# Kernel tuning notes

Measured on AMD Instinct MI355X. Metric: run time of the kernel, lower is better.

The kernel has to match this reference:

```python
import jax, jax.numpy as jnp
import numpy as np

NC = 16       # class_nums
C = 128       # in_channel == EMBEND_DIM
NS = 8192     # support points
NQ = 30000    # query points
EPS = 1e-8


def setup_inputs() -> dict:
    key = jax.random.key(0)
    ks = jax.random.split(key, 7)
    support_features = jax.random.normal(ks[0], (NS, C), dtype=jnp.float32)
    support_labels = jax.random.randint(ks[1], (NS,), 0, NC)
    query_features = jax.random.normal(ks[2], (NQ, C), dtype=jnp.float32)
    # proj = Linear(2C+1 -> C) + ReLU + Linear(C -> 128)
    s1 = 1.0 / np.sqrt(2 * C + 1)
    W1 = jax.random.uniform(ks[3], (2 * C + 1, C), minval=-s1, maxval=s1, dtype=jnp.float32)
    b1 = jax.random.uniform(ks[4], (C,), minval=-s1, maxval=s1, dtype=jnp.float32)
    s2 = 1.0 / np.sqrt(C)
    W2 = jax.random.uniform(ks[5], (C, C), minval=-s2, maxval=s2, dtype=jnp.float32)
    b2 = jax.random.uniform(ks[6], (C,), minval=-s2, maxval=s2, dtype=jnp.float32)
    return {"support_features": support_features, "support_labels": support_labels,
            "query_features": query_features, "W1": W1, "b1": b1, "W2": W2, "b2": b2}


def _prototypes(support_features, support_labels):
    # fused scatter-mean replacing the per-class Python loop
    sums = jax.ops.segment_sum(support_features, support_labels, num_segments=NC)  # [Nc, C]
    counts = jax.ops.segment_sum(jnp.ones((support_features.shape[0],), support_features.dtype),
                                 support_labels, num_segments=NC)                   # [Nc]
    return jnp.where(counts[:, None] > 0, sums / jnp.maximum(counts, 1.0)[:, None], 0.0)


def reference(support_features, support_labels, query_features, W1, b1, W2, b2):
    protos = _prototypes(support_features, support_labels)                # [Nc, C]
    # MD_distance: cosine similarity between each query and each class prototype
    qn = query_features / jnp.maximum(jnp.linalg.norm(query_features, axis=-1, keepdims=True), EPS)
    pn = protos / jnp.maximum(jnp.linalg.norm(protos, axis=-1, keepdims=True), EPS)
    cos = jnp.einsum('qc,nc->qn', qn, pn)                                 # [Nq, Nc]
    # proj(cat([query, proto, cos], -1)) without materializing the [Nq,Nc,2C+1] concat:
    # split W1 rows into query part, proto part, and cos part.
    Wq, Wp, Wc = W1[:C], W1[C:2 * C], W1[2 * C]                           # [C,C],[C,C],[C]
    h = jax.nn.relu(jnp.einsum('qc,ch->qh', query_features, Wq)[:, None, :]
                    + jnp.einsum('nc,ch->nh', protos, Wp)[None, :, :]
                    + cos[:, :, None] * Wc[None, None, :]
                    + b1)                                                 # [Nq, Nc, C]
    similarity = jnp.einsum('qnh,ho->qno', h, W2) + b2                    # [Nq, Nc, 128]
    return similarity, cos[:, :, None]
```

## Files before the change

kernel.cpp:

```cpp
#include <hip/hip_runtime.h>

#define NQ_ 30000
#define NC_ 16
#define C_  128
#define NS_ 8192
#define QB  16
#define NBLK (NQ_/QB)

typedef __attribute__((ext_vector_type(4))) float  f32x4;
typedef __attribute__((ext_vector_type(8))) short  s16x8;

#define WS_PART  0
#define WS_PCNT  32768
#define WS_T     33024
#define WS_PACK  35072

__device__ inline short f2bf(float x){
  unsigned u = __float_as_uint(x);
  u += 0x7fffu + ((u >> 16) & 1u);
  return (short)(u >> 16);
}

__global__ __launch_bounds__(128) void protoA(const float* __restrict__ sf,
                                              const int* __restrict__ lbl,
                                              const float* __restrict__ W1,
                                              const float* __restrict__ W2,
                                              float* __restrict__ ws){
  const int b = blockIdx.x;
  const int t = threadIdx.x;
  if (b < 256){
    const int cls = b >> 4;
    const int ch  = b & 15;
    const int r0  = ch * (NS_/16);
    float s = 0.f; int cnt = 0;
    #pragma unroll 4
    for (int r = r0; r < r0 + NS_/16; ++r){
      if (lbl[r] == cls){ s += sf[(size_t)r*C_ + t]; ++cnt; }
    }
    ws[WS_PART + (cls*16 + ch)*C_ + t] = s;
    if (t == 0) ws[WS_PCNT + cls*16 + ch] = (float)cnt;
  } else {
    short* packo = (short*)(ws + WS_PACK);
    const int g0 = (b - 256)*1024 + t*8;
    const int gg = g0 & 16383;
    const int ln = (gg >> 3) & 63, ks = (gg >> 9) & 3, wvv = gg >> 11;
    const int kb = ks*32 + ((ln >> 4) & 3)*8;
    const int col = wvv*16 + (ln & 15);
    const float* src = (g0 < 16384) ? W2 : W1;
    s16x8 v;
    #pragma unroll
    for (int i = 0; i < 8; ++i) v[i] = f2bf(src[(size_t)(kb + i)*C_ + col]);
    *(s16x8*)&packo[g0] = v;
  }
}

__global__ __launch_bounds__(128) void protoB(const float* __restrict__ W1,
                                              const float* __restrict__ b1,
                                              float* __restrict__ ws){
  __shared__ float pr[C_];
  __shared__ float rns;
  const int n = blockIdx.x;
  const int h = threadIdx.x;
  float s = 0.f;
  #pragma unroll
  for (int ch = 0; ch < 16; ++ch) s += ws[WS_PART + (n*16 + ch)*C_ + h];
  float cnt = 0.f;
  #pragma unroll
  for (int ch = 0; ch < 16; ++ch) cnt += ws[WS_PCNT + n*16 + ch];
  const float pv = (cnt > 0.f) ? s / fmaxf(cnt, 1.f) : 0.f;
  pr[h] = pv;
  __syncthreads();
  if (h < 64){
    float q = pr[h]*pr[h] + pr[h+64]*pr[h+64];
    q += __shfl_xor(q, 1);  q += __shfl_xor(q, 2);  q += __shfl_xor(q, 4);
    q += __shfl_xor(q, 8);  q += __shfl_xor(q, 16); q += __shfl_xor(q, 32);
    if (h == 0) rns = 1.f / fmaxf(sqrtf(q), 1e-8f);
  }
  __syncthreads();
  {
    short* packo = (short*)(ws + WS_PACK);
    const int k = h;
    const int gg = ((k >> 5)*64 + ((k >> 3) & 3)*16 + n)*8 + (k & 7);
    packo[32768 + gg] = f2bf(pv * rns);
  }
  float acc = b1[h];
  #pragma unroll 8
  for (int c = 0; c < C_; ++c) acc = fmaf(pr[c], W1[(size_t)(C_ + c)*C_ + h], acc);
  ws[WS_T + n*C_ + h] = acc;
}

__global__ __launch_bounds__(256, 4) void fused_main(const float* __restrict__ qfeat,
                                                     const float* __restrict__ W1,
                                                     const float* __restrict__ b2,
                                                     const float* __restrict__ ws,
                                                     float* __restrict__ out){
  __shared__ __align__(16) char un[16384];
  __shared__ float qw[QB][132];
  __shared__ float tl16[NC_][132];
  __shared__ float cosl[QB][NC_];
  __shared__ float rqn[QB];
  __shared__ float wcl[C_];

  float (*qfs)[132] = (float(*)[132])un;
  short* hfrag = (short*)un;

  const int t    = threadIdx.x;
  const int lane = t & 63;
  const int wv   = t >> 6;
  const int fr   = lane & 15;
  const int fg   = lane >> 4;
  const int qbase = blockIdx.x * QB;
  float* out_cos = out + (size_t)NQ_ * NC_ * C_;
  const short* pack = (const short*)(ws + WS_PACK);

  {
    const int idx = t * 8, q = idx >> 7, c = idx & 127;
    *(f32x4*)&qfs[q][c]      = *(const f32x4*)(qfeat + (size_t)qbase*C_ + idx);
    *(f32x4*)&qfs[q][c+4]    = *(const f32x4*)(qfeat + (size_t)qbase*C_ + idx + 4);
    *(f32x4*)&tl16[q][c]     = *(const f32x4*)(ws + WS_T + idx);
    *(f32x4*)&tl16[q][c+4]   = *(const f32x4*)(ws + WS_T + idx + 4);
    if (t < 32) *(f32x4*)&wcl[t*4] = *(const f32x4*)(W1 + 2*C_*C_ + t*4);
  }
  __syncthreads();

  if (t < 128){
    int q = t >> 3; int c0 = (t & 7) * 16;
    float s = 0.f;
    #pragma unroll
    for (int m = 0; m < 16; ++m){ float v = qfs[q][c0+m]; s = fmaf(v, v, s); }
    s += __shfl_xor(s, 1); s += __shfl_xor(s, 2); s += __shfl_xor(s, 4);
    if ((t & 7) == 0) rqn[q] = 1.f / fmaxf(sqrtf(s), 1e-8f);
  }

  s16x8 qfr[4];
  #pragma unroll
  for (int ks = 0; ks < 4; ++ks){
    const int c0 = ks*32 + fg*8;
    f32x4 a = *(const f32x4*)&qfs[fr][c0];
    f32x4 b = *(const f32x4*)&qfs[fr][c0+4];
    s16x8 v;
    v[0]=f2bf(a[0]); v[1]=f2bf(a[1]); v[2]=f2bf(a[2]); v[3]=f2bf(a[3]);
    v[4]=f2bf(b[0]); v[5]=f2bf(b[1]); v[6]=f2bf(b[2]); v[7]=f2bf(b[3]);
    qfr[ks] = v;
  }
  s16x8 w2f[2][4];
  float b2v[2];
  #pragma unroll
  for (int j = 0; j < 2; ++j){
    const int tt = wv*2 + j;
    #pragma unroll
    for (int ks = 0; ks < 4; ++ks)
      w2f[j][ks] = *(const s16x8*)&pack[((tt*4 + ks)*64 + lane)*8];
    b2v[j] = b2[tt*16 + fr];
  }
  __syncthreads();

  #pragma unroll
  for (int j = 0; j < 2; ++j){
    const int tt = wv*2 + j;
    f32x4 dq = {0.f,0.f,0.f,0.f};
    #pragma unroll
    for (int ks = 0; ks < 4; ++ks)
      dq = __builtin_amdgcn_mfma_f32_16x16x32_bf16(qfr[ks],
             *(const s16x8*)&pack[16384 + ((tt*4 + ks)*64 + lane)*8], dq, 0,0,0);
    #pragma unroll
    for (int r = 0; r < 4; ++r) qw[fg*4 + r][tt*16 + fr] = dq[r];
  }
  if (wv == 0){
    f32x4 dc = {0.f,0.f,0.f,0.f};
    #pragma unroll
    for (int ks = 0; ks < 4; ++ks)
      dc = __builtin_amdgcn_mfma_f32_16x16x32_bf16(qfr[ks],
             *(const s16x8*)&pack[32768 + (ks*64 + lane)*8], dc, 0,0,0);
    #pragma unroll
    for (int r = 0; r < 4; ++r){
      const int q = fg*4 + r;
      const float cv = dc[r] * rqn[q];
      cosl[q][fr] = cv;
      out_cos[(size_t)(qbase + q)*NC_ + fr] = cv;
    }
  }
  __syncthreads();

  const int k0 = wv*32 + fg*8;
  const f32x4 t8a = *(const f32x4*)&tl16[fr][k0];
  const f32x4 t8b = *(const f32x4*)&tl16[fr][k0+4];
  const f32x4 w8a = *(const f32x4*)&wcl[k0];
  const f32x4 w8b = *(const f32x4*)&wcl[k0+4];

  #pragma unroll
  for (int chunk = 0; chunk < 4; ++chunk){
    const int q0 = chunk * 4;
    #pragma unroll
    for (int qq = 0; qq < 4; ++qq){
      const int q = q0 + qq;
      f32x4 qa = *(const f32x4*)&qw[q][k0];
      f32x4 qb = *(const f32x4*)&qw[q][k0+4];
      const float cv = cosl[q][fr];
      s16x8 hv;
      #pragma unroll
      for (int jj = 0; jj < 4; ++jj)
        hv[jj] = f2bf(fmaxf(fmaf(cv, w8a[jj], qa[jj] + t8a[jj]), 0.f));
      #pragma unroll
      for (int jj = 0; jj < 4; ++jj)
        hv[4+jj] = f2bf(fmaxf(fmaf(cv, w8b[jj], qb[jj] + t8b[jj]), 0.f));
      *(s16x8*)&hfrag[qq*2048 + wv*512 + lane*8] = hv;
    }
    __syncthreads();
    #pragma unroll
    for (int qq = 0; qq < 4; ++qq){
      const short* hb = &hfrag[qq*2048 + lane*8];
      s16x8 a0 = *(const s16x8*)&hb[0];
      s16x8 a1 = *(const s16x8*)&hb[512];
      s16x8 a2 = *(const s16x8*)&hb[1024];
      s16x8 a3 = *(const s16x8*)&hb[1536];
      const size_t qout = (size_t)(qbase + q0 + qq) * (NC_*C_);
      #pragma unroll
      for (int j = 0; j < 2; ++j){
        f32x4 acc = {b2v[j], b2v[j], b2v[j], b2v[j]};
        acc = __builtin_amdgcn_mfma_f32_16x16x32_bf16(a0, w2f[j][0], acc, 0,0,0);
        acc = __builtin_amdgcn_mfma_f32_16x16x32_bf16(a1, w2f[j][1], acc, 0,0,0);
        acc = __builtin_amdgcn_mfma_f32_16x16x32_bf16(a2, w2f[j][2], acc, 0,0,0);
        acc = __builtin_amdgcn_mfma_f32_16x16x32_bf16(a3, w2f[j][3], acc, 0,0,0);
        const int ocol = (wv*2 + j)*16 + fr;
        #pragma unroll
        for (int r = 0; r < 4; ++r)
          out[qout + (fg*4 + r)*C_ + ocol] = acc[r];
      }
    }
    __syncthreads();
  }
}

extern "C" void kernel_launch(void* const* d_in, const int* in_sizes, int n_in,
                              void* d_out, int out_size, void* d_ws, size_t ws_size,
                              hipStream_t stream){
  const float* sf  = (const float*)d_in[0];
  const int*   lbl = (const int*)  d_in[1];
  const float* qf  = (const float*)d_in[2];
  const float* W1  = (const float*)d_in[3];
  const float* b1  = (const float*)d_in[4];
  const float* W2  = (const float*)d_in[5];
  const float* b2  = (const float*)d_in[6];
  float* ws  = (float*)d_ws;
  float* out = (float*)d_out;

  protoA<<<288, 128, 0, stream>>>(sf, lbl, W1, W2, ws);
  protoB<<<NC_, 128, 0, stream>>>(W1, b1, ws);
  fused_main<<<NBLK, 256, 0, stream>>>(qf, W1, b2, ws, out);
}
```

Measured before the change: 88.39 us.

## Stage MFMA outputs in double-buffered LDS for coalesced vector stores

Each wave now builds its full-K A fragments for the second matmul directly in registers instead of exchanging h through shared memory. The accumulator tiles are written to a double-buffered LDS staging area, then written to global memory as contiguous 32-byte vector stores per thread, overlapping with compute of the next query pair. This targets the scattered scalar output stores that dominate this output-write-bound kernel. The larger shared footprint lowers the occupancy hint from 4 to 3 blocks per CU, and the h values are recomputed redundantly across waves.

```diff
diff --git a/kernel.cpp b/kernel.cpp
--- a/kernel.cpp
+++ b/kernel.cpp
@@ -89,20 +89,19 @@
   ws[WS_T + n*C_ + h] = acc;
 }
 
-__global__ __launch_bounds__(256, 4) void fused_main(const float* __restrict__ qfeat,
+__global__ __launch_bounds__(256, 3) void fused_main(const float* __restrict__ qfeat,
                                                      const float* __restrict__ W1,
                                                      const float* __restrict__ b2,
                                                      const float* __restrict__ ws,
                                                      float* __restrict__ out){
-  __shared__ __align__(16) char un[16384];
+  __shared__ __align__(16) float simb[2*2*16*132];
   __shared__ float qw[QB][132];
   __shared__ float tl16[NC_][132];
   __shared__ float cosl[QB][NC_];
   __shared__ float rqn[QB];
   __shared__ float wcl[C_];
 
-  float (*qfs)[132] = (float(*)[132])un;
-  short* hfrag = (short*)un;
+  float (*qfs)[132] = (float(*)[132])simb;
 
   const int t    = threadIdx.x;
   const int lane = t & 63;
@@ -182,54 +181,69 @@
   }
   __syncthreads();
 
-  const int k0 = wv*32 + fg*8;
-  const f32x4 t8a = *(const f32x4*)&tl16[fr][k0];
-  const f32x4 t8b = *(const f32x4*)&tl16[fr][k0+4];
-  const f32x4 w8a = *(const f32x4*)&wcl[k0];
-  const f32x4 w8b = *(const f32x4*)&wcl[k0+4];
-
-  #pragma unroll
-  for (int chunk = 0; chunk < 4; ++chunk){
-    const int q0 = chunk * 4;
-    #pragma unroll
-    for (int qq = 0; qq < 4; ++qq){
-      const int q = q0 + qq;
-      f32x4 qa = *(const f32x4*)&qw[q][k0];
-      f32x4 qb = *(const f32x4*)&qw[q][k0+4];
+  auto do_C = [&](int p){
+    float* sb = simb + (p & 1) * (2*16*132);
+    #pragma unroll
+    for (int qq = 0; qq < 2; ++qq){
+      const int q = p*2 + qq;
       const float cv = cosl[q][fr];
-      s16x8 hv;
+      s16x8 af[4];
       #pragma unroll
-      for (int jj = 0; jj < 4; ++jj)
-        hv[jj] = f2bf(fmaxf(fmaf(cv, w8a[jj], qa[jj] + t8a[jj]), 0.f));
-      #pragma unroll
-      for (int jj = 0; jj < 4; ++jj)
-        hv[4+jj] = f2bf(fmaxf(fmaf(cv, w8b[jj], qb[jj] + t8b[jj]), 0.f));
-      *(s16x8*)&hfrag[qq*2048 + wv*512 + lane*8] = hv;
-    }
-    __syncthreads();
-    #pragma unroll
-    for (int qq = 0; qq < 4; ++qq){
-      const short* hb = &hfrag[qq*2048 + lane*8];
-      s16x8 a0 = *(const s16x8*)&hb[0];
-      s16x8 a1 = *(const s16x8*)&hb[512];
-      s16x8 a2 = *(const s16x8*)&hb[1024];
-      s16x8 a3 = *(const s16x8*)&hb[1536];
-      const size_t qout = (size_t)(qbase + q0 + qq) * (NC_*C_);
+      for (int ks = 0; ks < 4; ++ks){
+        const int k0 = ks*32 + fg*8;
+        const f32x4 qa = *(const f32x4*)&qw[q][k0];
+        const f32x4 qb = *(const f32x4*)&qw[q][k0+4];
+        const f32x4 ta = *(const f32x4*)&tl16[fr][k0];
+        const f32x4 tb = *(const f32x4*)&tl16[fr][k0+4];
+        const f32x4 wa = *(const f32x4*)&wcl[k0];
+        const f32x4 wb = *(const f32x4*)&wcl[k0+4];
+        s16x8 v;
+        #pragma unroll
+        for (int jj = 0; jj < 4; ++jj)
+          v[jj]   = f2bf(fmaxf(fmaf(cv, wa[jj], qa[jj] + ta[jj]), 0.f));
+        #pragma unroll
+        for (int jj = 0; jj < 4; ++jj)
+          v[4+jj] = f2bf(fmaxf(fmaf(cv, wb[jj], qb[jj] + tb[jj]), 0.f));
+        af[ks] = v;
+      }
       #pragma unroll
       for (int j = 0; j < 2; ++j){
         f32x4 acc = {b2v[j], b2v[j], b2v[j], b2v[j]};
-        acc = __builtin_amdgcn_mfma_f32_16x16x32_bf16(a0, w2f[j][0], acc, 0,0,0);
-        acc = __builtin_amdgcn_mfma_f32_16x16x32_bf16(a1, w2f[j][1], acc, 0,0,0);
-        acc = __builtin_amdgcn_mfma_f32_16x16x32_bf16(a2, w2f[j][2], acc, 0,0,0);
-        acc = __builtin_amdgcn_mfma_f32_16x16x32_bf16(a3, w2f[j][3], acc, 0,0,0);
+        acc = __builtin_amdgcn_mfma_f32_16x16x32_bf16(af[0], w2f[j][0], acc, 0,0,0);
+        acc = __builtin_amdgcn_mfma_f32_16x16x32_bf16(af[1], w2f[j][1], acc, 0,0,0);
+        acc = __builtin_amdgcn_mfma_f32_16x16x32_bf16(af[2], w2f[j][2], acc, 0,0,0);
+        acc = __builtin_amdgcn_mfma_f32_16x16x32_bf16(af[3], w2f[j][3], acc, 0,0,0);
         const int ocol = (wv*2 + j)*16 + fr;
         #pragma unroll
         for (int r = 0; r < 4; ++r)
-          out[qout + (fg*4 + r)*C_ + ocol] = acc[r];
+          sb[(qq*16 + fg*4 + r)*132 + ocol] = acc[r];
       }
     }
+  };
+
+  auto do_ST = [&](int p){
+    const float* sb = simb + (p & 1) * (2*16*132);
+    const int n = t >> 4, o = (t & 15) * 8;
+    #pragma unroll
+    for (int qq = 0; qq < 2; ++qq){
+      const float* sp = &sb[(qq*16 + n)*132 + o];
+      const f32x4 v0 = *(const f32x4*)sp;
+      const f32x4 v1 = *(const f32x4*)(sp + 4);
+      float* dst = out + (size_t)(qbase + p*2 + qq)*(NC_*C_) + n*C_ + o;
+      *(f32x4*)dst       = v0;
+      *(f32x4*)(dst + 4) = v1;
+    }
+  };
+
+  do_C(0);
+  __syncthreads();
+  #pragma unroll
+  for (int p = 1; p < 8; ++p){
+    do_ST(p-1);
+    do_C(p);
     __syncthreads();
   }
+  do_ST(7);
 }
 
 extern "C" void kernel_launch(void* const* d_in, const int* in_sizes, int n_in,
```

Result: slower. 108.3 us (+22.5%).
